# Kernel optimization log

Hardware: AMD Instinct MI355X
Metric: run time of the kernel (lower is better)

Reference implementation:

```python
import jax, jax.numpy as jnp
import numpy as np
from jax import lax

S, B, C = 128, 32, 16
VW, VC = 100000, 100
DW, DC = 256, 64
HW, HC = 512, 128
T = 17


def setup_inputs():
    key = jax.random.key(0)
    it = iter(jax.random.split(key, 40))

    def p(shape, scale=0.05):
        return jax.random.normal(next(it), shape, jnp.float32) * scale

    inp = {}
    inp['sentence'] = jax.random.randint(next(it), (S, B), 2, VW)
    inp['char'] = jax.random.randint(next(it), (B, S, C), 2, VC)
    inp['tags'] = jax.random.randint(next(it), (S, B), 0, T)
    inp['W_we'] = p((VW, DW)).at[1].set(0.0)  # padding_idx=1 row zeroed
    inp['W_ce'] = p((VC, DC)).at[1].set(0.0)
    Hc2, Hw2 = HC // 2, HW // 2
    for d in ('f', 'b'):
        inp['c_Wih_' + d] = p((4 * Hc2, DC))
        inp['c_Whh_' + d] = p((4 * Hc2, Hc2))
        inp['c_b_' + d] = p((4 * Hc2,))
        inp['w_Wih_' + d] = p((4 * Hw2, DW + HC))
        inp['w_Whh_' + d] = p((4 * Hw2, Hw2))
        inp['w_b_' + d] = p((4 * Hw2,))
    inp['emit_W'] = p((T, HW))
    inp['emit_b'] = p((T,))
    inp['crf_trans'] = p((T, T), 0.1)
    inp['crf_start'] = p((T,), 0.1)
    inp['crf_end'] = p((T,), 0.1)
    return inp


def _lstm(xs, Wih, Whh, b):
    # xs: (L, N, D); torch gate order i,f,g,o
    H = Whh.shape[1]

    def step(carry, x):
        h, c = carry
        g = x @ Wih.T + h @ Whh.T + b
        i, f, gg, o = jnp.split(g, 4, axis=-1)
        c = jax.nn.sigmoid(f) * c + jax.nn.sigmoid(i) * jnp.tanh(gg)
        h = jax.nn.sigmoid(o) * jnp.tanh(c)
        return (h, c), h

    z = jnp.zeros((xs.shape[1], H), xs.dtype)
    (hT, _), hs = lax.scan(step, (z, z), xs)
    return hs, hT


def _bilstm(xs, Wf, Uf, bf, Wb, Ub, bb):
    hs_f, hT_f = _lstm(xs, Wf, Uf, bf)
    hs_b, hT_b = _lstm(xs[::-1], Wb, Ub, bb)
    return jnp.concatenate([hs_f, hs_b[::-1]], axis=-1), hT_f, hT_b


def _crf_nll(em, tags, mask, trans, start, end):
    # em: (S,B,T); pytorch-crf log-likelihood, reduction='sum'; returns -llh
    b_idx = jnp.arange(em.shape[1])
    mf = mask.astype(em.dtype)
    score0 = start[tags[0]] + em[0, b_idx, tags[0]]

    def num_step(carry, inp):
        s, prev = carry
        e_t, t_t, m_t = inp
        s = s + (trans[prev, t_t] + e_t[b_idx, t_t]) * m_t
        prev = jnp.where(m_t > 0, t_t, prev)
        return (s, prev), None

    (num, last), _ = lax.scan(num_step, (score0, tags[0]), (em[1:], tags[1:], mf[1:]))
    num = num + end[last]

    alpha0 = start[None, :] + em[0]

    def den_step(alpha, inp):
        e_t, m_t = inp
        nxt = jax.scipy.special.logsumexp(alpha[:, :, None] + trans[None] + e_t[:, None, :], axis=1)
        return jnp.where(m_t[:, None] > 0, nxt, alpha), None

    alpha, _ = lax.scan(den_step, alpha0, (em[1:], mf[1:]))
    den = jax.scipy.special.logsumexp(alpha + end[None, :], axis=1)
    return -jnp.sum(num - den)


def reference(sentence, char, tags, W_we, W_ce, c_Wih_f, c_Whh_f, c_b_f, c_Wih_b, c_Whh_b, c_b_b, w_Wih_f, w_Whh_f, w_b_f, w_Wih_b, w_Whh_b, w_b_b, emit_W, emit_b, crf_trans, crf_start, crf_end):
    # char features: batch the per-position char BiLSTM across (B*S)
    ce = W_ce[char]  # (B,S,C,DC)
    ce = jnp.transpose(ce, (2, 0, 1, 3)).reshape(C, B * S, DC)
    _, hTf, hTb = _bilstm(ce, c_Wih_f, c_Whh_f, c_b_f, c_Wih_b, c_Whh_b, c_b_b)
    ch = jnp.concatenate([hTf, hTb], axis=-1).reshape(B, S, HC).transpose(1, 0, 2)  # (S,B,HC)
    x = jnp.concatenate([ch, W_we[sentence]], axis=-1)  # (S,B,HC+DW)
    out, _, _ = _bilstm(x, w_Wih_f, w_Whh_f, w_b_f, w_Wih_b, w_Whh_b, w_b_b)  # (S,B,HW)
    em = out @ emit_W.T + emit_b  # (S,B,T)
    mask = sentence != 1
    return _crf_nll(em, tags, mask, crf_trans, crf_start, crf_end)
```

## Files before the change

kernel.cpp:

```cpp
#include <hip/hip_runtime.h>
#include <math.h>

#define SS 128
#define BB 32
#define CC 16
#define DW 256
#define DC 64
#define HC 128
#define KX 384
#define TT 17

typedef __attribute__((ext_vector_type(8))) short bf16x8;
typedef __attribute__((ext_vector_type(4))) float f32x4;
typedef unsigned long long ull_t;

__device__ __forceinline__ float sigf(float x) { return 1.0f / (1.0f + __expf(-x)); }
__device__ __forceinline__ float tanhfast(float x) {
  float xc = fminf(fmaxf(x, -15.f), 15.f);
  float e = __expf(2.f * xc);
  return (e - 1.f) / (e + 1.f);
}
__device__ __forceinline__ unsigned short f2bf(float x) {
  unsigned int u = __float_as_uint(x);
  u += 0x7FFF + ((u >> 16) & 1);
  return (unsigned short)(u >> 16);
}
__device__ __forceinline__ unsigned ld_u32(const unsigned* p) {
  return __hip_atomic_load(p, __ATOMIC_RELAXED, __HIP_MEMORY_SCOPE_AGENT);
}
__device__ __forceinline__ void st_u32(unsigned* p, unsigned v) {
  __hip_atomic_store(p, v, __ATOMIC_RELAXED, __HIP_MEMORY_SCOPE_AGENT);
}
__device__ __forceinline__ ull_t ld_ull(const ull_t* p) {
  return __hip_atomic_load(p, __ATOMIC_RELAXED, __HIP_MEMORY_SCOPE_AGENT);
}
__device__ __forceinline__ void st_ull(ull_t* p, ull_t v) {
  __hip_atomic_store(p, v, __ATOMIC_RELAXED, __HIP_MEMORY_SCOPE_AGENT);
}

__global__ __launch_bounds__(256) void k0_ihvocab(
    const float* __restrict__ Wce,
    const float* __restrict__ WihF, const float* __restrict__ bF,
    const float* __restrict__ WihB, const float* __restrict__ bB,
    float* __restrict__ ihv) {
  int blk = blockIdx.x;
  int d = blk / 100, v = blk % 100;
  const float* Wih = d ? WihB : WihF;
  const float* bb  = d ? bB   : bF;
  __shared__ float ce[DC];
  if (threadIdx.x < DC) ce[threadIdx.x] = Wce[v * DC + threadIdx.x];
  __syncthreads();
  int g = threadIdx.x;
  float acc = bb[g];
  #pragma unroll 16
  for (int k = 0; k < DC; ++k) acc += ce[k] * Wih[g * DC + k];
  ihv[(d * 100 + v) * 256 + g] = acc;
}

__global__ __launch_bounds__(256) void k1_char(
    const int* __restrict__ charidx,
    const float* __restrict__ WhhF, const float* __restrict__ WhhB,
    const float* __restrict__ ihv,
    float* __restrict__ x)
{
  int blk = blockIdx.x;
  int d = blk >> 8;
  int n0 = (blk & 255) * 16;
  const float* Whh = d ? WhhB : WhhF;

  __shared__ float Wl[256 * 68];
  __shared__ float hl[16 * 68];

  for (int i = threadIdx.x; i < 256 * 64; i += 256) {
    int g = i >> 6, k = i & 63;
    Wl[g * 68 + k] = Whh[i];
  }
  __syncthreads();

  int hh = threadIdx.x & 63;
  int ng = threadIdx.x >> 6;
  float c[4] = {0.f, 0.f, 0.f, 0.f};
  float h[4] = {0.f, 0.f, 0.f, 0.f};
  int bb_[4], ss_[4];
  #pragma unroll
  for (int m = 0; m < 4; ++m) {
    int n = n0 + ng + 4 * m;
    bb_[m] = n >> 7; ss_[m] = n & 127;
  }

  for (int t = 0; t < CC; ++t) {
    int cpos = d ? (CC - 1 - t) : t;
    float acc[4][4];
    #pragma unroll
    for (int m = 0; m < 4; ++m) {
      int v = charidx[bb_[m] * (SS * CC) + ss_[m] * CC + cpos];
      const float* base = ihv + (d * 100 + v) * 256 + hh;
      acc[m][0] = base[0]; acc[m][1] = base[64]; acc[m][2] = base[128]; acc[m][3] = base[192];
    }
    if (t > 0) {
      #pragma unroll 4
      for (int k = 0; k < 64; k += 4) {
        float4 w4[4];
        #pragma unroll
        for (int q = 0; q < 4; ++q)
          w4[q] = *(const float4*)&Wl[(q * 64 + hh) * 68 + k];
        #pragma unroll
        for (int m = 0; m < 4; ++m) {
          float4 h4 = *(const float4*)&hl[(ng + 4 * m) * 68 + k];
          #pragma unroll
          for (int q = 0; q < 4; ++q)
            acc[m][q] += h4.x * w4[q].x + h4.y * w4[q].y + h4.z * w4[q].z + h4.w * w4[q].w;
        }
      }
      __syncthreads();
    }
    #pragma unroll
    for (int m = 0; m < 4; ++m) {
      float ig = sigf(acc[m][0]);
      float fg = sigf(acc[m][1]);
      float gg = tanhfast(acc[m][2]);
      float og = sigf(acc[m][3]);
      c[m] = fg * c[m] + ig * gg;
      h[m] = og * tanhfast(c[m]);
      hl[(ng + 4 * m) * 68 + hh] = h[m];
    }
    __syncthreads();
  }
  #pragma unroll
  for (int m = 0; m < 4; ++m) {
    int row = ss_[m] * BB + bb_[m];
    x[row * KX + d * 64 + hh] = h[m];
  }
}

__global__ __launch_bounds__(64) void k2_we(
    const int* __restrict__ sentence, const float* __restrict__ Wwe,
    float* __restrict__ x) {
  int row = blockIdx.x;
  int idx = sentence[row];
  const float4* src = (const float4*)(Wwe + (size_t)idx * DW);
  float4* dst = (float4*)(x + (size_t)row * KX + HC);
  dst[threadIdx.x] = src[threadIdx.x];
}

__global__ __launch_bounds__(256) void k3_ihgemm(
    const float* __restrict__ x,
    const float* __restrict__ WihF, const float* __restrict__ bF,
    const float* __restrict__ WihB, const float* __restrict__ bB,
    float* __restrict__ wg) {
  int n0 = blockIdx.x * 128;
  int m0 = blockIdx.y * 128;
  int d  = n0 >> 10;
  int gb = n0 & 1023;
  const float* Wih  = d ? WihB : WihF;
  const float* bias = d ? bB   : bF;

  __shared__ float At[32][132];
  __shared__ float Bt[32][132];

  int tid = threadIdx.x;
  int half = tid & 1, r = tid >> 1;
  int tm = tid & 15, tn = tid >> 4;
  float acc[8][8] = {};

  for (int k0 = 0; k0 < KX; k0 += 32) {
    __syncthreads();
    {
      const float4* srcA = (const float4*)(x + (size_t)(m0 + r) * KX + k0 + half * 16);
      const float4* srcB = (const float4*)(Wih + (size_t)(gb + r) * KX + k0 + half * 16);
      #pragma unroll
      for (int q = 0; q < 4; ++q) {
        float4 v = srcA[q];
        int kk = half * 16 + q * 4;
        At[kk + 0][r] = v.x; At[kk + 1][r] = v.y; At[kk + 2][r] = v.z; At[kk + 3][r] = v.w;
      }
      #pragma unroll
      for (int q = 0; q < 4; ++q) {
        float4 v = srcB[q];
        int kk = half * 16 + q * 4;
        Bt[kk + 0][r] = v.x; Bt[kk + 1][r] = v.y; Bt[kk + 2][r] = v.z; Bt[kk + 3][r] = v.w;
      }
    }
    __syncthreads();
    #pragma unroll 8
    for (int k = 0; k < 32; ++k) {
      float4 a0 = *(const float4*)&At[k][tm * 8];
      float4 a1 = *(const float4*)&At[k][tm * 8 + 4];
      float4 b0 = *(const float4*)&Bt[k][tn * 8];
      float4 b1 = *(const float4*)&Bt[k][tn * 8 + 4];
      float av[8] = {a0.x, a0.y, a0.z, a0.w, a1.x, a1.y, a1.z, a1.w};
      float bv[8] = {b0.x, b0.y, b0.z, b0.w, b1.x, b1.y, b1.z, b1.w};
      #pragma unroll
      for (int i = 0; i < 8; ++i)
        #pragma unroll
        for (int jq = 0; jq < 8; ++jq)
          acc[i][jq] += av[i] * bv[jq];
    }
  }
  float bv8[8];
  #pragma unroll
  for (int jq = 0; jq < 8; ++jq) bv8[jq] = bias[gb + tn * 8 + jq];
  #pragma unroll
  for (int i = 0; i < 8; ++i) {
    int m = m0 + tm * 8 + i;
    float* dst = wg + ((size_t)(d * 4096 + m)) * 1024 + gb + tn * 8;
    float4 v0 = {acc[i][0] + bv8[0], acc[i][1] + bv8[1], acc[i][2] + bv8[2], acc[i][3] + bv8[3]};
    float4 v1 = {acc[i][4] + bv8[4], acc[i][5] + bv8[5], acc[i][6] + bv8[6], acc[i][7] + bv8[7]};
    *(float4*)dst = v0; *(float4*)(dst + 4) = v1;
  }
}

__global__ __launch_bounds__(64, 1) void k4_word(
    const float* __restrict__ WhhF, const float* __restrict__ WhhB,
    const float* __restrict__ wg,
    float* __restrict__ outh,
    unsigned short* __restrict__ hbuf,
    unsigned int* __restrict__ flags) {
  const int blk = blockIdx.x;
  const int d = blk >> 4, widx = blk & 15;
  const int l = threadIdx.x;
  const int l15 = l & 15, q4 = l >> 4;
  const int j0w = widx * 16;
  const float* __restrict__ Whh = d ? WhhB : WhhF;
  unsigned short* hb_d = hbuf + d * 16384;
  unsigned int* fl = flags + d * 16;

  __shared__ unsigned short hl[32 * 24];

  bf16x8 Bf[4][8];
  #pragma unroll
  for (int q = 0; q < 4; ++q) {
    const float* wr = Whh + (size_t)(q * 256 + j0w + l15) * 256 + q4 * 8;
    #pragma unroll
    for (int ks = 0; ks < 8; ++ks) {
      float4 lo = *(const float4*)(wr + ks * 32);
      float4 hi = *(const float4*)(wr + ks * 32 + 4);
      bf16x8 f;
      f[0] = (short)f2bf(lo.x); f[1] = (short)f2bf(lo.y);
      f[2] = (short)f2bf(lo.z); f[3] = (short)f2bf(lo.w);
      f[4] = (short)f2bf(hi.x); f[5] = (short)f2bf(hi.y);
      f[6] = (short)f2bf(hi.z); f[7] = (short)f2bf(hi.w);
      Bf[q][ks] = f;
    }
  }

  float cst[8];
  #pragma unroll
  for (int i = 0; i < 8; ++i) cst[i] = 0.f;

  const int rb = l >> 1;
  const int rh = l & 1;

  for (int t = 0; t < SS; ++t) {
    const int s = d ? (SS - 1 - t) : t;

    f32x4 acc[4][2];
    const float* wgs = wg + ((size_t)d * 4096 + (size_t)s * 32) * 1024 + j0w + l15;
    #pragma unroll
    for (int q = 0; q < 4; ++q)
      #pragma unroll
      for (int mt = 0; mt < 2; ++mt)
        #pragma unroll
        for (int r = 0; r < 4; ++r)
          acc[q][mt][r] = wgs[(size_t)(q4 * 4 + r + mt * 16) * 1024 + q * 256];

    if (t > 0) {
      for (;;) {
        unsigned tg = ld_u32(fl + l15);
        if (__all((int)(tg >= (unsigned)t))) break;
        __builtin_amdgcn_s_sleep(1);
      }

      const unsigned short* hp = hb_d + ((t - 1) & 1) * 8192 + q4 * 8;
      bf16x8 Af[2][8];
      #pragma unroll
      for (int mt = 0; mt < 2; ++mt)
        #pragma unroll
        for (int ks = 0; ks < 8; ++ks) {
          const ull_t* p = (const ull_t*)(hp + (size_t)(l15 + mt * 16) * 256 + ks * 32);
          union { ull_t u[2]; bf16x8 v; } cvt;
          cvt.u[0] = ld_ull(p);
          cvt.u[1] = ld_ull(p + 1);
          Af[mt][ks] = cvt.v;
        }
      #pragma unroll
      for (int q = 0; q < 4; ++q)
        #pragma unroll
        for (int mt = 0; mt < 2; ++mt) {
          f32x4 c = acc[q][mt];
          #pragma unroll
          for (int ks = 0; ks < 8; ++ks)
            c = __builtin_amdgcn_mfma_f32_16x16x32_bf16(Af[mt][ks], Bf[q][ks], c, 0, 0, 0);
          acc[q][mt] = c;
        }
    }

    float hv[8];
    #pragma unroll
    for (int mt = 0; mt < 2; ++mt)
      #pragma unroll
      for (int r = 0; r < 4; ++r) {
        int ix = mt * 4 + r;
        float ig = sigf(acc[0][mt][r]);
        float fg = sigf(acc[1][mt][r]);
        float gg = tanhfast(acc[2][mt][r]);
        float og = sigf(acc[3][mt][r]);
        float c2 = fg * cst[ix] + ig * gg;
        cst[ix] = c2;
        hv[ix] = og * tanhfast(c2);
      }

    #pragma unroll
    for (int mt = 0; mt < 2; ++mt)
      #pragma unroll
      for (int r = 0; r < 4; ++r)
        hl[(q4 * 4 + r + mt * 16) * 24 + l15] = f2bf(hv[mt * 4 + r]);
    ull_t plo = *(const ull_t*)&hl[rb * 24 + rh * 8];
    ull_t phi = *(const ull_t*)&hl[rb * 24 + rh * 8 + 4];
    ull_t* dst = (ull_t*)(hb_d + (t & 1) * 8192 + (size_t)rb * 256 + j0w + rh * 8);
    st_ull(dst, plo);
    st_ull(dst + 1, phi);
    asm volatile("s_waitcnt vmcnt(0)" ::: "memory");
    if (l == 0) st_u32(fl + widx, (unsigned)(t + 1));

    float* op = outh + (size_t)(s * 32) * 512 + d * 256 + j0w + l15;
    #pragma unroll
    for (int mt = 0; mt < 2; ++mt)
      #pragma unroll
      for (int r = 0; r < 4; ++r)
        __builtin_nontemporal_store(hv[mt * 4 + r], op + (size_t)(q4 * 4 + r + mt * 16) * 512);
  }
}

__global__ __launch_bounds__(64) void k5_emit(
    const float* __restrict__ outh, const float* __restrict__ eW,
    const float* __restrict__ eb, float* __restrict__ em) {
  int row = blockIdx.x;
  int t = threadIdx.x;
  if (t < TT) {
    const float4* o4 = (const float4*)(outh + (size_t)row * 512);
    const float4* w4 = (const float4*)(eW + (size_t)t * 512);
    float acc = 0.f;
    #pragma unroll 16
    for (int k = 0; k < 128; ++k) {
      float4 a = o4[k], bq = w4[k];
      acc += a.x * bq.x + a.y * bq.y + a.z * bq.z + a.w * bq.w;
    }
    em[row * TT + t] = acc + eb[t];
  }
}

__global__ __launch_bounds__(64) void k6_crf(
    const int* __restrict__ sentence, const int* __restrict__ tags,
    const float* __restrict__ em, const float* __restrict__ trans,
    const float* __restrict__ startv, const float* __restrict__ endv,
    float* __restrict__ outp) {
  int b = blockIdx.x;
  int j = threadIdx.x;
  __shared__ float ash[TT];
  __shared__ float red[TT];
  float tc[TT];
  float alpha = 0.f;
  if (j < TT) {
    #pragma unroll
    for (int i = 0; i < TT; ++i) tc[i] = trans[i * TT + j];
    alpha = startv[j] + em[(0 * BB + b) * TT + j];
  }
  for (int s = 1; s < SS; ++s) {
    if (j < TT) ash[j] = alpha;
    __syncthreads();
    int m = (sentence[s * BB + b] != 1) ? 1 : 0;
    if (j < TT) {
      float mx = -1e30f;
      #pragma unroll
      for (int i = 0; i < TT; ++i) mx = fmaxf(mx, ash[i] + tc[i]);
      float sum = 0.f;
      #pragma unroll
      for (int i = 0; i < TT; ++i) sum += __expf(ash[i] + tc[i] - mx);
      float nxt = mx + __logf(sum) + em[(s * BB + b) * TT + j];
      if (m) alpha = nxt;
    }
    __syncthreads();
  }
  if (j < TT) red[j] = alpha + endv[j];
  __syncthreads();
  if (j == 0) {
    float mx = -1e30f;
    for (int i = 0; i < TT; ++i) mx = fmaxf(mx, red[i]);
    float sum = 0.f;
    for (int i = 0; i < TT; ++i) sum += __expf(red[i] - mx);
    float den = mx + __logf(sum);
    int prev = tags[0 * BB + b];
    float num = startv[prev] + em[(0 * BB + b) * TT + prev];
    for (int s = 1; s < SS; ++s) {
      int tg = tags[s * BB + b];
      if (sentence[s * BB + b] != 1) {
        num += trans[prev * TT + tg] + em[(s * BB + b) * TT + tg];
        prev = tg;
      }
    }
    num += endv[prev];
    atomicAdd(outp, den - num);
  }
}

extern "C" void kernel_launch(void* const* d_in, const int* in_sizes, int n_in,
                              void* d_out, int out_size, void* d_ws, size_t ws_size,
                              hipStream_t stream) {
  (void)in_sizes; (void)n_in; (void)out_size; (void)ws_size;
  const int*   sentence = (const int*)d_in[0];
  const int*   charidx  = (const int*)d_in[1];
  const int*   tags     = (const int*)d_in[2];
  const float* Wwe   = (const float*)d_in[3];
  const float* Wce   = (const float*)d_in[4];
  const float* cWihF = (const float*)d_in[5];
  const float* cWhhF = (const float*)d_in[6];
  const float* cbF   = (const float*)d_in[7];
  const float* wWihF = (const float*)d_in[8];
  const float* wWhhF = (const float*)d_in[9];
  const float* wbF   = (const float*)d_in[10];
  const float* cWihB = (const float*)d_in[11];
  const float* cWhhB = (const float*)d_in[12];
  const float* cbB   = (const float*)d_in[13];
  const float* wWihB = (const float*)d_in[14];
  const float* wWhhB = (const float*)d_in[15];
  const float* wbB   = (const float*)d_in[16];
  const float* eW    = (const float*)d_in[17];
  const float* eb    = (const float*)d_in[18];
  const float* trans = (const float*)d_in[19];
  const float* startv= (const float*)d_in[20];
  const float* endv  = (const float*)d_in[21];

  char* ws = (char*)d_ws;
  unsigned int*   flags = (unsigned int*)(ws + 0);
  float*          ihv   = (float*)(ws + 512);
  float*          x     = (float*)(ws + 205312);
  float*          wg    = (float*)(ws + 6496768);
  unsigned short* hbuf  = (unsigned short*)(ws + 40051200);
  float*          outh  = (float*)(ws + 40116736);
  float*          em    = (float*)(ws + 48505344);

  hipMemsetAsync(flags, 0, 512, stream);
  hipMemsetAsync(d_out, 0, sizeof(float), stream);

  k0_ihvocab<<<200, 256, 0, stream>>>(Wce, cWihF, cbF, cWihB, cbB, ihv);
  k1_char<<<512, 256, 0, stream>>>(charidx, cWhhF, cWhhB, ihv, x);
  k2_we<<<4096, 64, 0, stream>>>(sentence, Wwe, x);
  k3_ihgemm<<<dim3(16, 32), 256, 0, stream>>>(x, wWihF, wbF, wWihB, wbB, wg);
  k4_word<<<32, 64, 0, stream>>>(wWhhF, wWhhB, wg, outh, hbuf, flags);
  k5_emit<<<4096, 64, 0, stream>>>(outh, eW, eb, em);
  k6_crf<<<32, 64, 0, stream>>>(sentence, tags, em, trans, startv, endv, (float*)d_out);
}
```

Measured before the change: 1.019 ms.

## Replace flag-based step sync with step-tagged hidden-state words in word LSTM

The word BiLSTM recurrence now packs each bf16 hidden value with a 16-bit step tag into a 32-bit word. Consumers spin on the data itself, checking tags, instead of polling separate per-block flags. This removes the LDS staging, the vmcnt wait before the flag store, and the extra flag round trip on each of the 128 serial steps. In exchange the hidden-state buffer doubles in size, every poll reloads the full operand set, and the buffer is placed at the same workspace offset as the emission scratch, which k5 overwrites after k4 finishes.

```diff
diff --git a/kernel.cpp b/kernel.cpp
--- a/kernel.cpp
+++ b/kernel.cpp
@@ -25,17 +25,11 @@
   u += 0x7FFF + ((u >> 16) & 1);
   return (unsigned short)(u >> 16);
 }
-__device__ __forceinline__ unsigned ld_u32(const unsigned* p) {
-  return __hip_atomic_load(p, __ATOMIC_RELAXED, __HIP_MEMORY_SCOPE_AGENT);
-}
 __device__ __forceinline__ void st_u32(unsigned* p, unsigned v) {
   __hip_atomic_store(p, v, __ATOMIC_RELAXED, __HIP_MEMORY_SCOPE_AGENT);
 }
 __device__ __forceinline__ ull_t ld_ull(const ull_t* p) {
   return __hip_atomic_load(p, __ATOMIC_RELAXED, __HIP_MEMORY_SCOPE_AGENT);
-}
-__device__ __forceinline__ void st_ull(ull_t* p, ull_t v) {
-  __hip_atomic_store(p, v, __ATOMIC_RELAXED, __HIP_MEMORY_SCOPE_AGENT);
 }
 
 __global__ __launch_bounds__(256) void k0_ihvocab(
@@ -214,18 +208,14 @@
     const float* __restrict__ WhhF, const float* __restrict__ WhhB,
     const float* __restrict__ wg,
     float* __restrict__ outh,
-    unsigned short* __restrict__ hbuf,
-    unsigned int* __restrict__ flags) {
+    unsigned int* __restrict__ hbuf) {
   const int blk = blockIdx.x;
   const int d = blk >> 4, widx = blk & 15;
   const int l = threadIdx.x;
   const int l15 = l & 15, q4 = l >> 4;
   const int j0w = widx * 16;
   const float* __restrict__ Whh = d ? WhhB : WhhF;
-  unsigned short* hb_d = hbuf + d * 16384;
-  unsigned int* fl = flags + d * 16;
-
-  __shared__ unsigned short hl[32 * 24];
+  unsigned int* hb_d = hbuf + d * 16384;
 
   bf16x8 Bf[4][8];
   #pragma unroll
@@ -248,9 +238,6 @@
   #pragma unroll
   for (int i = 0; i < 8; ++i) cst[i] = 0.f;
 
-  const int rb = l >> 1;
-  const int rh = l & 1;
-
   for (int t = 0; t < SS; ++t) {
     const int s = d ? (SS - 1 - t) : t;
 
@@ -265,24 +252,28 @@
           acc[q][mt][r] = wgs[(size_t)(q4 * 4 + r + mt * 16) * 1024 + q * 256];
 
     if (t > 0) {
+      const unsigned int* hp = hb_d + ((t - 1) & 1) * 8192;
+      const ull_t want2 = ((ull_t)(unsigned)t << 16) | ((ull_t)(unsigned)t << 48);
+      bf16x8 Af[2][8];
       for (;;) {
-        unsigned tg = ld_u32(fl + l15);
-        if (__all((int)(tg >= (unsigned)t))) break;
-        __builtin_amdgcn_s_sleep(1);
-      }
-
-      const unsigned short* hp = hb_d + ((t - 1) & 1) * 8192 + q4 * 8;
-      bf16x8 Af[2][8];
-      #pragma unroll
-      for (int mt = 0; mt < 2; ++mt)
-        #pragma unroll
-        for (int ks = 0; ks < 8; ++ks) {
-          const ull_t* p = (const ull_t*)(hp + (size_t)(l15 + mt * 16) * 256 + ks * 32);
-          union { ull_t u[2]; bf16x8 v; } cvt;
-          cvt.u[0] = ld_ull(p);
-          cvt.u[1] = ld_ull(p + 1);
-          Af[mt][ks] = cvt.v;
+        ull_t bad = 0;
+        #pragma unroll
+        for (int mt = 0; mt < 2; ++mt) {
+          const ull_t* rp = (const ull_t*)(hp + (size_t)(l15 + mt * 16) * 256) + q4 * 4;
+          #pragma unroll
+          for (int ks = 0; ks < 8; ++ks) {
+            union { unsigned int u[4]; bf16x8 v; } cv;
+            #pragma unroll
+            for (int p = 0; p < 4; ++p) {
+              ull_t w = ld_ull(rp + ks * 16 + p);
+              bad |= (w ^ want2) & 0xffff0000ffff0000ull;
+              cv.u[p] = (unsigned)((w & 0xffffull) | ((w >> 16) & 0xffff0000ull));
+            }
+            Af[mt][ks] = cv.v;
+          }
         }
+        if (__all(bad == 0)) break;
+      }
       #pragma unroll
       for (int q = 0; q < 4; ++q)
         #pragma unroll
@@ -310,18 +301,18 @@
         hv[ix] = og * tanhfast(c2);
       }
 
-    #pragma unroll
-    for (int mt = 0; mt < 2; ++mt)
-      #pragma unroll
-      for (int r = 0; r < 4; ++r)
-        hl[(q4 * 4 + r + mt * 16) * 24 + l15] = f2bf(hv[mt * 4 + r]);
-    ull_t plo = *(const ull_t*)&hl[rb * 24 + rh * 8];
-    ull_t phi = *(const ull_t*)&hl[rb * 24 + rh * 8 + 4];
-    ull_t* dst = (ull_t*)(hb_d + (t & 1) * 8192 + (size_t)rb * 256 + j0w + rh * 8);
-    st_ull(dst, plo);
-    st_ull(dst + 1, phi);
-    asm volatile("s_waitcnt vmcnt(0)" ::: "memory");
-    if (l == 0) st_u32(fl + widx, (unsigned)(t + 1));
+    {
+      unsigned int tagv = ((unsigned)(t + 1)) << 16;
+      unsigned int* wp = hb_d + (t & 1) * 8192;
+      #pragma unroll
+      for (int mt = 0; mt < 2; ++mt)
+        #pragma unroll
+        for (int r = 0; r < 4; ++r) {
+          int row = q4 * 4 + r + mt * 16;
+          st_u32(wp + (size_t)row * 256 + j0w + l15,
+                 tagv | (unsigned)f2bf(hv[mt * 4 + r]));
+        }
+    }
 
     float* op = outh + (size_t)(s * 32) * 512 + d * 256 + j0w + l15;
     #pragma unroll
@@ -432,22 +423,21 @@
   const float* endv  = (const float*)d_in[21];
 
   char* ws = (char*)d_ws;
-  unsigned int*   flags = (unsigned int*)(ws + 0);
   float*          ihv   = (float*)(ws + 512);
   float*          x     = (float*)(ws + 205312);
   float*          wg    = (float*)(ws + 6496768);
-  unsigned short* hbuf  = (unsigned short*)(ws + 40051200);
   float*          outh  = (float*)(ws + 40116736);
   float*          em    = (float*)(ws + 48505344);
-
-  hipMemsetAsync(flags, 0, 512, stream);
+  unsigned int*   hbuf  = (unsigned int*)(ws + 48505344);
+
+  hipMemsetAsync(hbuf, 0, 131072, stream);
   hipMemsetAsync(d_out, 0, sizeof(float), stream);
 
   k0_ihvocab<<<200, 256, 0, stream>>>(Wce, cWihF, cbF, cWihB, cbB, ihv);
   k1_char<<<512, 256, 0, stream>>>(charidx, cWhhF, cWhhB, ihv, x);
   k2_we<<<4096, 64, 0, stream>>>(sentence, Wwe, x);
   k3_ihgemm<<<dim3(16, 32), 256, 0, stream>>>(x, wWihF, wbF, wWihB, wbB, wg);
-  k4_word<<<32, 64, 0, stream>>>(wWhhF, wWhhB, wg, outh, hbuf, flags);
+  k4_word<<<32, 64, 0, stream>>>(wWhhF, wWhhB, wg, outh, hbuf);
   k5_emit<<<4096, 64, 0, stream>>>(outh, eW, eb, em);
   k6_crf<<<32, 64, 0, stream>>>(sentence, tags, em, trans, startv, endv, (float*)d_out);
 }
```

Measured after the change: 1.248 ms. 22.4% more time.
